# Optimization experiments

Measured on AMD Instinct MI355X. Metric: run time of the kernel, lower is better.

Reference implementation:

```python
import jax, jax.numpy as jnp
import numpy as np

N_NODES = 100000
N_EDGES = 3200000
N_FEAT = 512
HIDDEN = 16
OUT_DIM = 1


def setup_inputs() -> dict:
    key = jax.random.key(0)
    ks = jax.random.split(key, 6)
    x = jax.random.normal(ks[0], (N_NODES, N_FEAT), dtype=jnp.float32)
    lap_vals = jax.random.uniform(ks[1], (N_EDGES,), dtype=jnp.float32)
    W1 = jax.random.normal(ks[2], (N_FEAT, HIDDEN), dtype=jnp.float32) * 0.05
    b1 = jnp.zeros((HIDDEN,), dtype=jnp.float32)
    W2 = jax.random.normal(ks[3], (HIDDEN, OUT_DIM), dtype=jnp.float32) * 0.05
    b2 = jnp.zeros((OUT_DIM,), dtype=jnp.float32)
    lap_rows = jax.random.randint(ks[4], (N_EDGES,), 0, N_NODES, dtype=jnp.int32)
    lap_cols = jax.random.randint(ks[5], (N_EDGES,), 0, N_NODES, dtype=jnp.int32)
    return {"x": x, "lap_vals": lap_vals, "W1": W1, "b1": b1,
            "W2": W2, "b2": b2, "lap_rows": lap_rows, "lap_cols": lap_cols}


def _spmm(vals, rows, cols, dense):
    # COO sparse [N,N] @ dense [N,D]: gather source rows, scale, scatter-add.
    return jax.ops.segment_sum(vals[:, None] * dense[cols], rows,
                               num_segments=N_NODES)


def reference(x, lap_vals, W1, b1, W2, b2, lap_rows, lap_cols):
    # Layer 1: dense GEMM -> sparse aggregation -> fused bias + relu
    h = jax.nn.relu(_spmm(lap_vals, lap_rows, lap_cols, x @ W1) + b1)
    # Layer 2: dense GEMM -> sparse aggregation -> fused bias + sigmoid
    out = jax.nn.sigmoid(_spmm(lap_vals, lap_rows, lap_cols, h @ W2) + b2)
    return out
```

## Files before the change

### kernel.cpp

```cpp
#include <hip/hip_runtime.h>
#include <cstdint>
#include <cstddef>

#define N_NODES 100000
#define N_EDGES 3200000
#define N_FEAT  512
#define HIDDEN  16
#define NBUCK   ((N_NODES + 127) / 128)
#define BCAP    4608
#define CHUNK   2048
#define NGB     ((N_NODES + 63) / 64)
#define NBS     ((N_EDGES + CHUNK - 1) / CHUNK)
#define AGG_T   512

static_assert(NGB == NBS, "parity interleave requires equal role counts");

__device__ __forceinline__ void gload_lds16(const float* g, void* lds) {
  __builtin_amdgcn_global_load_lds(
      (const __attribute__((address_space(1))) void*)g,
      (__attribute__((address_space(3))) void*)lds, 16, 0, 0);
}

__global__ __launch_bounds__(256)
void k_prep(int* __restrict__ cursor) {
  const int i = blockIdx.x * 256 + threadIdx.x;
  if (i < NBUCK) cursor[i] = 0;
}

__global__ __launch_bounds__(256)
void k_mega2(const float* __restrict__ x, const float* __restrict__ W1,
             float* __restrict__ xw, const int* __restrict__ rows,
             const int* __restrict__ cols, const float* __restrict__ vals,
             int* __restrict__ cursor, int2* __restrict__ binned) {
  __shared__ __align__(16) char smem[32768];
  const int t = threadIdx.x;

  if ((blockIdx.x & 1) == 0) {
    float4 (*xs)[2][256] = reinterpret_cast<float4 (*)[2][256]>(smem);
    const int l = t & 63;
    const int w = __builtin_amdgcn_readfirstlane(t >> 6);
    const int rbase = (blockIdx.x >> 1) * 64;
    const int kbase0 = w * 128;

    float acc[16];
#pragma unroll
    for (int c = 0; c < 16; ++c) acc[c] = 0.f;

    const int sq   = ((l & 3) ^ ((l >> 3) & 3)) * 4;
    const int srow = l >> 2;

    auto STAGE = [&](int b, int ck) {
      const int kb = kbase0 + ck * 16;
#pragma unroll
      for (int i = 0; i < 4; ++i) {
        int grow = rbase + i * 16 + srow;
        if (grow >= N_NODES) grow = N_NODES - 1;
        gload_lds16(x + (size_t)grow * N_FEAT + kb + sq, &xs[w][b][i * 64]);
      }
    };

    const int rsw = (l >> 1) & 3;
    auto COMPUTE = [&](int b, int ck) {
      const int kb = kbase0 + ck * 16;
#pragma unroll
      for (int q = 0; q < 4; ++q) {
        float4 xv = xs[w][b][l * 4 + (q ^ rsw)];
        float xe[4] = {xv.x, xv.y, xv.z, xv.w};
#pragma unroll
        for (int j = 0; j < 4; ++j) {
          const float* wrow = W1 + (size_t)(kb + q * 4 + j) * 16;
#pragma unroll
          for (int c = 0; c < 16; ++c)
            acc[c] = fmaf(xe[j], wrow[c], acc[c]);
        }
      }
    };

    STAGE(0, 0);
#pragma unroll 1
    for (int ck = 0; ck < 8; ++ck) {
      const int b = ck & 1;
      if (ck + 1 < 8) {
        STAGE(b ^ 1, ck + 1);
        asm volatile("s_waitcnt vmcnt(4)" ::: "memory");
      } else {
        asm volatile("s_waitcnt vmcnt(0)" ::: "memory");
      }
      COMPUTE(b, ck);
    }

    float4* red = &xs[w][0][0];
    red[l * 4 + 0] = make_float4(acc[0],  acc[1],  acc[2],  acc[3]);
    red[l * 4 + 1] = make_float4(acc[4],  acc[5],  acc[6],  acc[7]);
    red[l * 4 + 2] = make_float4(acc[8],  acc[9],  acc[10], acc[11]);
    red[l * 4 + 3] = make_float4(acc[12], acc[13], acc[14], acc[15]);
    __syncthreads();

    const int rr = t >> 2, qq = t & 3;
    const int grow = rbase + rr;
    if (grow < N_NODES) {
      const int s = rr * 4 + qq;
      float4 a = xs[0][0][s], b4 = xs[1][0][s], c4 = xs[2][0][s], d4 = xs[3][0][s];
      float4 o = make_float4(a.x + b4.x + c4.x + d4.x, a.y + b4.y + c4.y + d4.y,
                             a.z + b4.z + c4.z + d4.z, a.w + b4.w + c4.w + d4.w);
      ((float4*)xw)[(size_t)grow * 4 + qq] = o;
    }
  } else {
    int* hist = (int*)smem;
    const int e0 = (blockIdx.x >> 1) * CHUNK;
    const int nv = (N_EDGES - e0 < CHUNK) ? (N_EDGES - e0) : CHUNK;

    for (int b = t; b < NBUCK; b += 256) hist[b] = 0;
    __syncthreads();

    for (int i = t; i < nv; i += 256)
      atomicAdd(&hist[rows[e0 + i] >> 7], 1);
    __syncthreads();

    for (int b = t; b < NBUCK; b += 256) {
      const int h = hist[b];
      hist[b] = (h > 0) ? atomicAdd(&cursor[b], h) : 0;
    }
    __syncthreads();

    for (int i = t; i < nv; i += 256) {
      const int e = e0 + i;
      const int r = rows[e];
      const int b = r >> 7;
      const int off = atomicAdd(&hist[b], 1);
      if (off < BCAP)
        binned[(size_t)b * BCAP + off] =
            make_int2(cols[e] | ((r & 127) << 20), __float_as_int(vals[e]));
    }
  }
}

__global__ __launch_bounds__(AGG_T)
void k_sortagg(const int2* __restrict__ binned, const int* __restrict__ cursor,
               int2* __restrict__ binned2, int* __restrict__ row_beg,
               int* __restrict__ row_end, const float* __restrict__ xw,
               const float* __restrict__ b1, const float* __restrict__ W2,
               float* __restrict__ hw1) {
  __shared__ int2 stash[BCAP];
  __shared__ int hist[128];
  __shared__ int inc[128];
  __shared__ int cnt2[128];
  const int t = threadIdx.x;
  const int b = blockIdx.x;
  const int raw = cursor[b];
  const int cnt = raw < BCAP ? raw : BCAP;
  const int2* ep = binned + (size_t)b * BCAP;

  if (t < 128) { hist[t] = 0; cnt2[t] = 0; }
  __syncthreads();

  for (int i = t; i < cnt; i += AGG_T)
    atomicAdd(&hist[(ep[i].x >> 20) & 127], 1);
  __syncthreads();

  if (t < 128) inc[t] = hist[t];
  __syncthreads();
#pragma unroll
  for (int off = 1; off < 128; off <<= 1) {
    int add = (t >= off && t < 128) ? inc[t - off] : 0;
    __syncthreads();
    if (t < 128) inc[t] += add;
    __syncthreads();
  }

  if (t < 128) {
    const int r = b * 128 + t;
    if (r < N_NODES) {
      row_beg[r] = b * BCAP + inc[t] - hist[t];
      row_end[r] = b * BCAP + inc[t];
    }
  }

  for (int i = t; i < cnt; i += AGG_T) {
    const int2 e = ep[i];
    const int row = (e.x >> 20) & 127;
    const int off = inc[row] - hist[row] + atomicAdd(&cnt2[row], 1);
    stash[off] = e;
  }
  __syncthreads();

  int2* eq = binned2 + (size_t)b * BCAP;
  for (int i = t; i < cnt; i += AGG_T) eq[i] = stash[i];

  const int lane16 = t & 15;
  const int g = t >> 4;
  const float bb = b1[lane16];
  const float ww = W2[lane16];
#pragma unroll 1
  for (int rr = g; rr < 128; rr += 32) {
    const int r = b * 128 + rr;
    if (r >= N_NODES) continue;
    const int s = inc[rr] - hist[rr], e2 = inc[rr];
    float a0 = 0.f, a1 = 0.f, a2 = 0.f, a3 = 0.f;
    int i = s;
    for (; i + 3 < e2; i += 4) {
      int2 ea = stash[i],     eb = stash[i + 1];
      int2 ec = stash[i + 2], ed = stash[i + 3];
      a0 = fmaf(__int_as_float(ea.y), xw[(size_t)(ea.x & 0xFFFFF) * 16 + lane16], a0);
      a1 = fmaf(__int_as_float(eb.y), xw[(size_t)(eb.x & 0xFFFFF) * 16 + lane16], a1);
      a2 = fmaf(__int_as_float(ec.y), xw[(size_t)(ec.x & 0xFFFFF) * 16 + lane16], a2);
      a3 = fmaf(__int_as_float(ed.y), xw[(size_t)(ed.x & 0xFFFFF) * 16 + lane16], a3);
    }
    for (; i < e2; ++i) {
      int2 ea = stash[i];
      a0 = fmaf(__int_as_float(ea.y), xw[(size_t)(ea.x & 0xFFFFF) * 16 + lane16], a0);
    }
    float h = fmaxf((a0 + a1) + (a2 + a3) + bb, 0.f);
    float p = h * ww;
#pragma unroll
    for (int m = 8; m >= 1; m >>= 1) p += __shfl_xor(p, m, 16);
    if (lane16 == 0) hw1[r] = p;
  }
}

__global__ __launch_bounds__(256)
void k_fused2(const int2* __restrict__ binned2, const int* __restrict__ row_beg,
              const int* __restrict__ row_end, const float* __restrict__ hw1,
              const float* __restrict__ b2, float* __restrict__ out) {
  const int t = threadIdx.x;
  const int lane16 = t & 15;
  const int r = blockIdx.x * 16 + (t >> 4);
  if (r >= N_NODES) return;
  const int s = row_beg[r], e = row_end[r];
  float acc = 0.f;
  for (int i = s + lane16; i < e; i += 16) {
    int2 ev = binned2[i];
    acc = fmaf(__int_as_float(ev.y), hw1[ev.x & 0xFFFFF], acc);
  }
#pragma unroll
  for (int m = 8; m >= 1; m >>= 1) acc += __shfl_xor(acc, m, 16);
  if (lane16 == 0) out[r] = 1.f / (1.f + expf(-(acc + b2[0])));
}

extern "C" void kernel_launch(void* const* d_in, const int* in_sizes, int n_in,
                              void* d_out, int out_size, void* d_ws, size_t ws_size,
                              hipStream_t stream) {
  const float* x    = (const float*)d_in[0];
  const float* vals = (const float*)d_in[1];
  const float* W1   = (const float*)d_in[2];
  const float* b1   = (const float*)d_in[3];
  const float* W2   = (const float*)d_in[4];
  const float* b2   = (const float*)d_in[5];
  const int*   rows = (const int*)d_in[6];
  const int*   cols = (const int*)d_in[7];
  float* out = (float*)d_out;

  char* w = (char*)d_ws;
  float* xw      = (float*)w;  w += (size_t)N_NODES * 16 * 4;
  int2*  binned  = (int2*)w;   w += (size_t)NBUCK * BCAP * 8;
  int2*  binned2 = (int2*)w;   w += (size_t)NBUCK * BCAP * 8;
  int*   cursor  = (int*)w;    w += (size_t)((NBUCK + 3) & ~3) * 4;
  int*   row_beg = (int*)w;    w += (size_t)N_NODES * 4;
  int*   row_end = (int*)w;    w += (size_t)N_NODES * 4;
  float* hw1     = (float*)w;

  k_prep    <<<(NBUCK + 255) / 256, 256,   0, stream>>>(cursor);
  k_mega2   <<<NGB + NBS,           256,   0, stream>>>(x, W1, xw, rows, cols,
                                                        vals, cursor, binned);
  k_sortagg <<<NBUCK,               AGG_T, 0, stream>>>(binned, cursor, binned2,
                                                        row_beg, row_end, xw,
                                                        b1, W2, hw1);
  k_fused2  <<<(N_NODES + 15) / 16, 256,   0, stream>>>(binned2, row_beg, row_end,
                                                        hw1, b2, out);
}
```

Measured before the change: 190.4 us.

## Double per-block work in fused GEMM/binning kernel and batch edge loads

Each GEMM block now processes two 64-row tiles and each binning block handles 4096 edges, halving the grid to 2*782 blocks. The scatter phase loads four edges per thread before doing the LDS atomics, using a separate base array so loads can be issued together and overlap. The LDS reduction buffer is XOR-swizzled to reduce bank conflicts. Fewer, heavier blocks cut launch and per-block setup overhead and global cursor atomics, at some cost in parallelism and tail balance.

```diff
diff --git a/kernel.cpp b/kernel.cpp
--- a/kernel.cpp
+++ b/kernel.cpp
@@ -8,12 +8,12 @@
 #define HIDDEN  16
 #define NBUCK   ((N_NODES + 127) / 128)
 #define BCAP    4608
-#define CHUNK   2048
-#define NGB     ((N_NODES + 63) / 64)
-#define NBS     ((N_EDGES + CHUNK - 1) / CHUNK)
+#define ECHUNK  4096
+#define NROLE   782
 #define AGG_T   512
 
-static_assert(NGB == NBS, "parity interleave requires equal role counts");
+static_assert((size_t)NROLE * ECHUNK >= N_EDGES, "edge coverage");
+static_assert((size_t)NROLE * 2 * 64 >= N_NODES, "row coverage");
 
 __device__ __forceinline__ void gload_lds16(const float* g, void* lds) {
   __builtin_amdgcn_global_load_lds(
@@ -39,76 +39,81 @@
     float4 (*xs)[2][256] = reinterpret_cast<float4 (*)[2][256]>(smem);
     const int l = t & 63;
     const int w = __builtin_amdgcn_readfirstlane(t >> 6);
-    const int rbase = (blockIdx.x >> 1) * 64;
     const int kbase0 = w * 128;
-
-    float acc[16];
-#pragma unroll
-    for (int c = 0; c < 16; ++c) acc[c] = 0.f;
-
     const int sq   = ((l & 3) ^ ((l >> 3) & 3)) * 4;
     const int srow = l >> 2;
-
-    auto STAGE = [&](int b, int ck) {
-      const int kb = kbase0 + ck * 16;
-#pragma unroll
-      for (int i = 0; i < 4; ++i) {
-        int grow = rbase + i * 16 + srow;
-        if (grow >= N_NODES) grow = N_NODES - 1;
-        gload_lds16(x + (size_t)grow * N_FEAT + kb + sq, &xs[w][b][i * 64]);
-      }
-    };
-
-    const int rsw = (l >> 1) & 3;
-    auto COMPUTE = [&](int b, int ck) {
-      const int kb = kbase0 + ck * 16;
-#pragma unroll
-      for (int q = 0; q < 4; ++q) {
-        float4 xv = xs[w][b][l * 4 + (q ^ rsw)];
-        float xe[4] = {xv.x, xv.y, xv.z, xv.w};
-#pragma unroll
-        for (int j = 0; j < 4; ++j) {
-          const float* wrow = W1 + (size_t)(kb + q * 4 + j) * 16;
-#pragma unroll
-          for (int c = 0; c < 16; ++c)
-            acc[c] = fmaf(xe[j], wrow[c], acc[c]);
+    const int rsw  = (l >> 1) & 3;
+
+#pragma unroll 1
+    for (int tile = 0; tile < 2; ++tile) {
+      const int rbase = ((blockIdx.x >> 1) * 2 + tile) * 64;
+
+      float acc[16];
+#pragma unroll
+      for (int c = 0; c < 16; ++c) acc[c] = 0.f;
+
+      auto STAGE = [&](int b, int ck) {
+        const int kb = kbase0 + ck * 16;
+#pragma unroll
+        for (int i = 0; i < 4; ++i) {
+          int grow = rbase + i * 16 + srow;
+          if (grow >= N_NODES) grow = N_NODES - 1;
+          gload_lds16(x + (size_t)grow * N_FEAT + kb + sq, &xs[w][b][i * 64]);
         }
-      }
-    };
-
-    STAGE(0, 0);
+      };
+
+      auto COMPUTE = [&](int b, int ck) {
+        const int kb = kbase0 + ck * 16;
+#pragma unroll
+        for (int q = 0; q < 4; ++q) {
+          float4 xv = xs[w][b][l * 4 + (q ^ rsw)];
+          float xe[4] = {xv.x, xv.y, xv.z, xv.w};
+#pragma unroll
+          for (int j = 0; j < 4; ++j) {
+            const float* wrow = W1 + (size_t)(kb + q * 4 + j) * 16;
+#pragma unroll
+            for (int c = 0; c < 16; ++c)
+              acc[c] = fmaf(xe[j], wrow[c], acc[c]);
+          }
+        }
+      };
+
+      STAGE(0, 0);
 #pragma unroll 1
-    for (int ck = 0; ck < 8; ++ck) {
-      const int b = ck & 1;
-      if (ck + 1 < 8) {
-        STAGE(b ^ 1, ck + 1);
-        asm volatile("s_waitcnt vmcnt(4)" ::: "memory");
-      } else {
-        asm volatile("s_waitcnt vmcnt(0)" ::: "memory");
-      }
-      COMPUTE(b, ck);
-    }
-
-    float4* red = &xs[w][0][0];
-    red[l * 4 + 0] = make_float4(acc[0],  acc[1],  acc[2],  acc[3]);
-    red[l * 4 + 1] = make_float4(acc[4],  acc[5],  acc[6],  acc[7]);
-    red[l * 4 + 2] = make_float4(acc[8],  acc[9],  acc[10], acc[11]);
-    red[l * 4 + 3] = make_float4(acc[12], acc[13], acc[14], acc[15]);
-    __syncthreads();
-
-    const int rr = t >> 2, qq = t & 3;
-    const int grow = rbase + rr;
-    if (grow < N_NODES) {
-      const int s = rr * 4 + qq;
-      float4 a = xs[0][0][s], b4 = xs[1][0][s], c4 = xs[2][0][s], d4 = xs[3][0][s];
-      float4 o = make_float4(a.x + b4.x + c4.x + d4.x, a.y + b4.y + c4.y + d4.y,
-                             a.z + b4.z + c4.z + d4.z, a.w + b4.w + c4.w + d4.w);
-      ((float4*)xw)[(size_t)grow * 4 + qq] = o;
+      for (int ck = 0; ck < 8; ++ck) {
+        const int b = ck & 1;
+        if (ck + 1 < 8) {
+          STAGE(b ^ 1, ck + 1);
+          asm volatile("s_waitcnt vmcnt(4)" ::: "memory");
+        } else {
+          asm volatile("s_waitcnt vmcnt(0)" ::: "memory");
+        }
+        COMPUTE(b, ck);
+      }
+
+      float4* red = &xs[w][0][0];
+      red[l * 4 + (0 ^ rsw)] = make_float4(acc[0],  acc[1],  acc[2],  acc[3]);
+      red[l * 4 + (1 ^ rsw)] = make_float4(acc[4],  acc[5],  acc[6],  acc[7]);
+      red[l * 4 + (2 ^ rsw)] = make_float4(acc[8],  acc[9],  acc[10], acc[11]);
+      red[l * 4 + (3 ^ rsw)] = make_float4(acc[12], acc[13], acc[14], acc[15]);
+      __syncthreads();
+
+      const int rr = t >> 2, qq = t & 3;
+      const int grow = rbase + rr;
+      if (grow < N_NODES) {
+        const int s = rr * 4 + (qq ^ ((rr >> 1) & 3));
+        float4 a = xs[0][0][s], b4 = xs[1][0][s], c4 = xs[2][0][s], d4 = xs[3][0][s];
+        float4 o = make_float4(a.x + b4.x + c4.x + d4.x, a.y + b4.y + c4.y + d4.y,
+                               a.z + b4.z + c4.z + d4.z, a.w + b4.w + c4.w + d4.w);
+        ((float4*)xw)[(size_t)grow * 4 + qq] = o;
+      }
+      __syncthreads();
     }
   } else {
     int* hist = (int*)smem;
-    const int e0 = (blockIdx.x >> 1) * CHUNK;
-    const int nv = (N_EDGES - e0 < CHUNK) ? (N_EDGES - e0) : CHUNK;
+    int* base = hist + NBUCK;
+    const int e0 = (blockIdx.x >> 1) * ECHUNK;
+    const int nv = (N_EDGES - e0 < ECHUNK) ? (N_EDGES - e0) : ECHUNK;
 
     for (int b = t; b < NBUCK; b += 256) hist[b] = 0;
     __syncthreads();
@@ -119,18 +124,58 @@
 
     for (int b = t; b < NBUCK; b += 256) {
       const int h = hist[b];
-      hist[b] = (h > 0) ? atomicAdd(&cursor[b], h) : 0;
-    }
-    __syncthreads();
-
-    for (int i = t; i < nv; i += 256) {
-      const int e = e0 + i;
-      const int r = rows[e];
-      const int b = r >> 7;
-      const int off = atomicAdd(&hist[b], 1);
-      if (off < BCAP)
-        binned[(size_t)b * BCAP + off] =
-            make_int2(cols[e] | ((r & 127) << 20), __float_as_int(vals[e]));
+      base[b] = (h > 0) ? atomicAdd(&cursor[b], h) : 0;
+      hist[b] = 0;
+    }
+    __syncthreads();
+
+#pragma unroll 1
+    for (int g0 = 0; g0 < nv; g0 += 1024) {
+      int2 ed0, ed1, ed2, ed3;
+      int  bk0, bk1, bk2, bk3;
+      const int i0 = g0 + 0 * 256 + t, i1 = g0 + 1 * 256 + t;
+      const int i2 = g0 + 2 * 256 + t, i3 = g0 + 3 * 256 + t;
+      const bool v0 = i0 < nv, v1 = i1 < nv, v2 = i2 < nv, v3 = i3 < nv;
+      {
+        const int e = e0 + (v0 ? i0 : 0);
+        const int r = rows[e];
+        ed0 = make_int2(cols[e] | ((r & 127) << 20), __float_as_int(vals[e]));
+        bk0 = r >> 7;
+      }
+      {
+        const int e = e0 + (v1 ? i1 : 0);
+        const int r = rows[e];
+        ed1 = make_int2(cols[e] | ((r & 127) << 20), __float_as_int(vals[e]));
+        bk1 = r >> 7;
+      }
+      {
+        const int e = e0 + (v2 ? i2 : 0);
+        const int r = rows[e];
+        ed2 = make_int2(cols[e] | ((r & 127) << 20), __float_as_int(vals[e]));
+        bk2 = r >> 7;
+      }
+      {
+        const int e = e0 + (v3 ? i3 : 0);
+        const int r = rows[e];
+        ed3 = make_int2(cols[e] | ((r & 127) << 20), __float_as_int(vals[e]));
+        bk3 = r >> 7;
+      }
+      if (v0) {
+        const int off = base[bk0] + atomicAdd(&hist[bk0], 1);
+        if (off < BCAP) binned[(size_t)bk0 * BCAP + off] = ed0;
+      }
+      if (v1) {
+        const int off = base[bk1] + atomicAdd(&hist[bk1], 1);
+        if (off < BCAP) binned[(size_t)bk1 * BCAP + off] = ed1;
+      }
+      if (v2) {
+        const int off = base[bk2] + atomicAdd(&hist[bk2], 1);
+        if (off < BCAP) binned[(size_t)bk2 * BCAP + off] = ed2;
+      }
+      if (v3) {
+        const int off = base[bk3] + atomicAdd(&hist[bk3], 1);
+        if (off < BCAP) binned[(size_t)bk3 * BCAP + off] = ed3;
+      }
     }
   }
 }
@@ -260,7 +305,7 @@
   float* hw1     = (float*)w;
 
   k_prep    <<<(NBUCK + 255) / 256, 256,   0, stream>>>(cursor);
-  k_mega2   <<<NGB + NBS,           256,   0, stream>>>(x, W1, xw, rows, cols,
+  k_mega2   <<<2 * NROLE,           256,   0, stream>>>(x, W1, xw, rows, cols,
                                                         vals, cursor, binned);
   k_sortagg <<<NBUCK,               AGG_T, 0, stream>>>(binned, cursor, binned2,
                                                         row_beg, row_end, xw,
```

Result: faster. 174.1 us (-8.5%).
